# Performance work log

Hardware: AMD Instinct MI355X
Metric: run time of the kernel (lower is better)

The kernel has to match this reference:

```python
import jax, jax.numpy as jnp
import numpy as np

N_HEADS = 16


def setup_inputs() -> dict:
    key = jax.random.key(0)
    ks = jax.random.split(key, 7)
    B, S, D = 2, 2048, 1024
    x = jax.random.normal(ks[0], (B, S, D), dtype=jnp.float32)
    attn_mask = jax.random.normal(ks[1], (S, S), dtype=jnp.float32) * 0.1
    attn_bias = jax.random.normal(ks[2], (B, S, S), dtype=jnp.float32) * 0.1
    Wqkv = jax.random.normal(ks[3], (D, 3 * D), dtype=jnp.float32) * (D ** -0.5)
    bqkv = jnp.zeros((3 * D,), dtype=jnp.float32)
    Wout = jax.random.normal(ks[4], (D, D), dtype=jnp.float32) * (D ** -0.5)
    bout = jnp.zeros((D,), dtype=jnp.float32)
    return {"x": x, "attn_mask": attn_mask, "attn_bias": attn_bias,
            "Wqkv": Wqkv, "bqkv": bqkv, "Wout": Wout, "bout": bout}


def reference(x, attn_mask, attn_bias, Wqkv, bqkv, Wout, bout):
    B, S, D = x.shape
    H = N_HEADS
    hd = D // H
    # qkv projection: [B,S,3D] -> [3,B,H,S,hd]
    qkv = (x @ Wqkv + bqkv).reshape(B, S, 3, H, hd).transpose(2, 0, 3, 1, 4)
    q, k, v = qkv[0], qkv[1], qkv[2]
    scores = jnp.einsum('bhqd,bhkd->bhqk', q, k) / (hd ** 0.5)
    scores = scores + attn_mask[None, None, :, :] + attn_bias[:, None, :, :]
    attn = jax.nn.softmax(scores, axis=-1)  # dropout p=0.0 (eval)
    out = jnp.einsum('bhqk,bhkd->bhqd', attn, v)
    out = out.transpose(0, 2, 1, 3).reshape(B, S, D)
    return out @ Wout + bout
```

## Files before the change

### kernel.cpp

```cpp
#include <hip/hip_runtime.h>
#include <hip/hip_bf16.h>


#define S_LEN 2048
#define DMODEL 1024
#define NH 16
#define HD 64

typedef __bf16 bf16x8 __attribute__((ext_vector_type(8)));
typedef __bf16 bf16x4 __attribute__((ext_vector_type(4)));
typedef __bf16 bf16x2v __attribute__((ext_vector_type(2)));
typedef float f32x4 __attribute__((ext_vector_type(4)));
typedef short s16x4 __attribute__((ext_vector_type(4)));

#define GLD_LDS16(g, l)                                              \
  __builtin_amdgcn_global_load_lds(                                  \
      (const __attribute__((address_space(1))) unsigned int*)(g),    \
      (__attribute__((address_space(3))) unsigned int*)(l), 16, 0, 0)

#if __has_builtin(__builtin_amdgcn_mfma_f32_16x16x16bf16_1k)
#define HAVE_MFMA_16x16x16_BF16 1
#else
#define HAVE_MFMA_16x16x16_BF16 0
#endif

__global__ __launch_bounds__(256) void cvt_x(const float* __restrict__ X,
                                             __bf16* __restrict__ Xb) {
  int i = blockIdx.x * 256 + threadIdx.x;
  float4 v = ((const float4*)X)[i];
  bf16x4 o = {(__bf16)v.x, (__bf16)v.y, (__bf16)v.z, (__bf16)v.w};
  *(bf16x4*)&Xb[(size_t)i * 4] = o;
}

__global__ __launch_bounds__(256) void cvt_wt(const float* __restrict__ W,
                                              __bf16* __restrict__ Wt,
                                              int ncols) {
  __shared__ float tile[64][65];
  const int n0 = blockIdx.x * 64;
  const int k0 = blockIdx.y * 64;
  const int tid = threadIdx.x;
  {
    int c = tid & 63, r4 = tid >> 6;
#pragma unroll
    for (int p = 0; p < 16; ++p) {
      int r = r4 + p * 4;
      tile[r][c] = W[(size_t)(k0 + r) * ncols + n0 + c];
    }
  }
  __syncthreads();
  {
    int cc = (tid & 31) * 2, r8 = tid >> 5;
#pragma unroll
    for (int p = 0; p < 8; ++p) {
      int rr = r8 + p * 8;
      bf16x2v o = {(__bf16)tile[cc][rr], (__bf16)tile[cc + 1][rr]};
      *(bf16x2v*)&Wt[(size_t)(n0 + rr) * 1024 + k0 + cc] = o;
    }
  }
}

__global__ __launch_bounds__(256) void mb_fuse(const float* __restrict__ mask,
                                               const float* __restrict__ bias,
                                               __bf16* __restrict__ MB) {
  const int kt = blockIdx.x, qt = blockIdx.y, b = blockIdx.z;
  const int tid = threadIdx.x;
  const int w = tid >> 6, lane = tid & 63;
  const int quad = lane >> 4, c = lane & 15;
  const size_t qrow = (size_t)(qt * 64 + w * 16 + c);
  const int col0 = kt * 64 + quad * 4;
  const float* mp = mask + qrow * S_LEN + col0;
  const float* bp = bias + (size_t)b * S_LEN * S_LEN + qrow * S_LEN + col0;
  __bf16 vals[16];
#pragma unroll
  for (int ct = 0; ct < 4; ++ct) {
    float4 m = *(const float4*)(mp + ct * 16);
    float4 a = *(const float4*)(bp + ct * 16);
    vals[ct * 4 + 0] = (__bf16)(m.x + a.x);
    vals[ct * 4 + 1] = (__bf16)(m.y + a.y);
    vals[ct * 4 + 2] = (__bf16)(m.z + a.z);
    vals[ct * 4 + 3] = (__bf16)(m.w + a.w);
  }
  __bf16* op =
      MB + (((size_t)(b * 32 + qt) * 32 + kt) * 4096) + (w * 64 + lane) * 16;
  *(bf16x8*)op = *(bf16x8*)&vals[0];
  *(bf16x8*)(op + 8) = *(bf16x8*)&vals[8];
}

__global__ __launch_bounds__(256) void gemm_qkv_mfma(
    const __bf16* __restrict__ Xb, const __bf16* __restrict__ Wt,
    const float* __restrict__ bqkv, __bf16* __restrict__ Qb,
    __bf16* __restrict__ Kb, __bf16* __restrict__ Vtb) {
  __shared__ __align__(16) __bf16 As[128 * 32];
  __shared__ __align__(16) __bf16 Bs[128 * 32];
  const int tid = threadIdx.x;
  const int w = tid >> 6, lane = tid & 63;
  const int c = lane & 15, quad = lane >> 4;
  const int wm = w >> 1, wn = w & 1;
  const int rowBase = blockIdx.y * 128;
  const int colBase = blockIdx.x * 128;

  f32x4 acc[4][4] = {};

  const __bf16* gA0 =
      Xb + (size_t)(rowBase + w * 32 + (lane >> 2)) * 1024 + (lane & 3) * 8;
  const __bf16* gB0 =
      Wt + (size_t)(colBase + w * 32 + (lane >> 2)) * 1024 + (lane & 3) * 8;
  __bf16* lA0 = &As[(w * 32) * 32];
  __bf16* lB0 = &Bs[(w * 32) * 32];

  for (int k0 = 0; k0 < 1024; k0 += 32) {
    __syncthreads();
#pragma unroll
    for (int p = 0; p < 2; ++p) {
      GLD_LDS16(gA0 + (size_t)p * 16 * 1024 + k0, lA0 + p * 16 * 32);
      GLD_LDS16(gB0 + (size_t)p * 16 * 1024 + k0, lB0 + p * 16 * 32);
    }
    __syncthreads();

    bf16x8 af[4], bfr[4];
#pragma unroll
    for (int mt = 0; mt < 4; ++mt)
      af[mt] = *(const bf16x8*)&As[(wm * 64 + mt * 16 + c) * 32 + quad * 8];
#pragma unroll
    for (int nt = 0; nt < 4; ++nt)
      bfr[nt] = *(const bf16x8*)&Bs[(wn * 64 + nt * 16 + c) * 32 + quad * 8];
#pragma unroll
    for (int mt = 0; mt < 4; ++mt)
#pragma unroll
      for (int nt = 0; nt < 4; ++nt)
        acc[mt][nt] = __builtin_amdgcn_mfma_f32_16x16x32_bf16(
            af[mt], bfr[nt], acc[mt][nt], 0, 0, 0);
  }

#pragma unroll
  for (int mt = 0; mt < 4; ++mt) {
    int row0 = rowBase + wm * 64 + mt * 16 + quad * 4;
#pragma unroll
    for (int nt = 0; nt < 4; ++nt) {
      int col = colBase + wn * 64 + nt * 16 + c;
      float bias = bqkv[col];
      int three = col >> 10;
      int h = (col & 1023) >> 6;
      int d = col & 63;
#pragma unroll
      for (int r = 0; r < 4; ++r) {
        int rr = row0 + r;
        int bb = rr >> 11, s = rr & 2047;
        float val = acc[mt][nt][r] + bias;
        size_t ho = (size_t)(bb * NH + h);
        if (three == 0)
          Qb[(ho * S_LEN + s) * HD + d] = (__bf16)val;
        else if (three == 1)
          Kb[(ho * S_LEN + s) * HD + d] = (__bf16)val;
        else
          Vtb[(ho * HD + d) * S_LEN + s] = (__bf16)val;
      }
    }
  }
}

__global__ __launch_bounds__(256) void attn_mfma(
    const __bf16* __restrict__ Qb, const __bf16* __restrict__ Kb,
    const __bf16* __restrict__ Vtb, const __bf16* __restrict__ MB,
    __bf16* __restrict__ AOb) {
  const int qt = blockIdx.x, h = blockIdx.y, b = blockIdx.z;
  const int tid = threadIdx.x;
  const int w = tid >> 6;
  const int lane = tid & 63;
  const int c = lane & 15;
  const int quad = lane >> 4;

  __shared__ __align__(16) __bf16 Ks[2][64 * 64];
  __shared__ __align__(16) __bf16 Vs[2][64 * 64];
#if !HAVE_MFMA_16x16x16_BF16
  __shared__ __align__(16) __bf16 P2[4][16 * 72];
#endif

  const int qbase = qt * 64;
  const size_t headoff = (size_t)(b * NH + h) * S_LEN * HD;
  const __bf16* Qg = Qb + headoff + (size_t)qbase * HD;
  const __bf16* Kg = Kb + headoff;
  const __bf16* Vg = Vtb + headoff;
  const __bf16* MBg = MB + ((size_t)(b * 32 + qt) * 32) * 4096;

  const int f0 = tid >> 3, f1 = f0 + 32;
  const int j = tid & 7;
  const int sj0 = j ^ (f0 & 7);
  const int sj1 = j ^ (f1 & 7);
  const int lds0 = tid * 8;
  const int lds1 = (256 + tid) * 8;

  bf16x8 qa0 = *(const bf16x8*)(Qg + (w * 16 + c) * HD + quad * 8);
  bf16x8 qa1 = *(const bf16x8*)(Qg + (w * 16 + c) * HD + quad * 8 + 32);

  const int rs0 = (quad ^ (c & 7)) * 8;
  const int rs1 = ((quad + 4) ^ (c & 7)) * 8;

  f32x4 Oa[4] = {};
  float lsum = 0.f;

  GLD_LDS16(Kg + (size_t)f0 * HD + sj0 * 8, &Ks[0][lds0]);
  GLD_LDS16(Kg + (size_t)f1 * HD + sj1 * 8, &Ks[0][lds1]);
  GLD_LDS16(Vg + (size_t)f0 * S_LEN + sj0 * 8, &Vs[0][lds0]);
  GLD_LDS16(Vg + (size_t)f1 * S_LEN + sj1 * 8, &Vs[0][lds1]);
  __syncthreads();

  for (int kt = 0; kt < 32; ++kt) {
    const int cur = kt & 1, nxt = cur ^ 1;
    const __bf16* MBl = MBg + (size_t)kt * 4096 + (w * 64 + lane) * 16;
    bf16x8 rMB0 = *(const bf16x8*)MBl;
    bf16x8 rMB1 = *(const bf16x8*)(MBl + 8);
    if (kt < 31) {
      const int kb1 = (kt + 1) * 64;
      GLD_LDS16(Kg + (size_t)(kb1 + f0) * HD + sj0 * 8, &Ks[nxt][lds0]);
      GLD_LDS16(Kg + (size_t)(kb1 + f1) * HD + sj1 * 8, &Ks[nxt][lds1]);
      GLD_LDS16(Vg + (size_t)f0 * S_LEN + kb1 + sj0 * 8, &Vs[nxt][lds0]);
      GLD_LDS16(Vg + (size_t)f1 * S_LEN + kb1 + sj1 * 8, &Vs[nxt][lds1]);
    }

    f32x4 sv[4];
#pragma unroll
    for (int ct = 0; ct < 4; ++ct) {
      f32x4 a = {};
      bf16x8 kf0 = *(const bf16x8*)&Ks[cur][(ct * 16 + c) * 64 + rs0];
      bf16x8 kf1 = *(const bf16x8*)&Ks[cur][(ct * 16 + c) * 64 + rs1];
      a = __builtin_amdgcn_mfma_f32_16x16x32_bf16(kf0, qa0, a, 0, 0, 0);
      a = __builtin_amdgcn_mfma_f32_16x16x32_bf16(kf1, qa1, a, 0, 0, 0);
      sv[ct] = a;
    }
    s16x4 pb[4];
#pragma unroll
    for (int ct = 0; ct < 4; ++ct) {
      __bf16 t4[4];
#pragma unroll
      for (int r = 0; r < 4; ++r) {
        float mb = (ct < 2) ? (float)rMB0[ct * 4 + r]
                            : (float)rMB1[(ct - 2) * 4 + r];
        float p = __expf(sv[ct][r] * 0.125f + mb - 8.0f);
        lsum += p;
        t4[r] = (__bf16)p;
      }
      pb[ct] = *(s16x4*)t4;
    }

#if HAVE_MFMA_16x16x16_BF16
#pragma unroll
    for (int ft = 0; ft < 4; ++ft) {
      const int fr = ft * 16 + c;
#pragma unroll
      for (int ct = 0; ct < 4; ++ct) {
        const int chunk = ((ct * 2 + (quad >> 1)) ^ (fr & 7)) * 8 +
                          (quad & 1) * 4;
        s16x4 vf = *(const s16x4*)&Vs[cur][fr * 64 + chunk];
        Oa[ft] = __builtin_amdgcn_mfma_f32_16x16x16bf16_1k(vf, pb[ct],
                                                           Oa[ft], 0, 0, 0);
      }
    }
#else
#pragma unroll
    for (int ct = 0; ct < 4; ++ct)
      *(bf16x4*)&P2[w][c * 72 + ct * 16 + quad * 4] = *(bf16x4*)&pb[ct];
    bf16x8 pf0 = *(const bf16x8*)&P2[w][c * 72 + quad * 8];
    bf16x8 pf1 = *(const bf16x8*)&P2[w][c * 72 + 32 + quad * 8];
#pragma unroll
    for (int ft = 0; ft < 4; ++ft) {
      const int fr = ft * 16 + c;
      bf16x8 vf0 = *(const bf16x8*)&Vs[cur][fr * 64 + rs0];
      bf16x8 vf1 = *(const bf16x8*)&Vs[cur][fr * 64 + rs1];
      Oa[ft] =
          __builtin_amdgcn_mfma_f32_16x16x32_bf16(vf0, pf0, Oa[ft], 0, 0, 0);
      Oa[ft] =
          __builtin_amdgcn_mfma_f32_16x16x32_bf16(vf1, pf1, Oa[ft], 0, 0, 0);
    }
#endif

    __syncthreads();
  }
  lsum += __shfl_xor(lsum, 16);
  lsum += __shfl_xor(lsum, 32);
  const float invl = 1.0f / lsum;
  __bf16* orow =
      AOb + (size_t)(b * S_LEN + qbase + w * 16 + c) * DMODEL + h * HD;
#pragma unroll
  for (int ft = 0; ft < 4; ++ft) {
    __bf16 t4[4];
#pragma unroll
    for (int r = 0; r < 4; ++r) t4[r] = (__bf16)(Oa[ft][r] * invl);
    *(bf16x4*)(orow + ft * 16 + quad * 4) = *(bf16x4*)t4;
  }
}

__global__ __launch_bounds__(256) void gemm_out_mfma(
    const __bf16* __restrict__ AOb, const __bf16* __restrict__ Wt2,
    const float* __restrict__ bout, float* __restrict__ Out) {
  __shared__ __align__(16) __bf16 As[128 * 32];
  __shared__ __align__(16) __bf16 Bs[128 * 32];
  const int tid = threadIdx.x;
  const int w = tid >> 6, lane = tid & 63;
  const int c = lane & 15, quad = lane >> 4;
  const int wm = w >> 1, wn = w & 1;
  const int rowBase = blockIdx.y * 128;
  const int colBase = blockIdx.x * 128;

  f32x4 acc[4][4] = {};

  const __bf16* gA0 =
      AOb + (size_t)(rowBase + w * 32 + (lane >> 2)) * 1024 + (lane & 3) * 8;
  const __bf16* gB0 =
      Wt2 + (size_t)(colBase + w * 32 + (lane >> 2)) * 1024 + (lane & 3) * 8;
  __bf16* lA0 = &As[(w * 32) * 32];
  __bf16* lB0 = &Bs[(w * 32) * 32];

  for (int k0 = 0; k0 < 1024; k0 += 32) {
    __syncthreads();
#pragma unroll
    for (int p = 0; p < 2; ++p) {
      GLD_LDS16(gA0 + (size_t)p * 16 * 1024 + k0, lA0 + p * 16 * 32);
      GLD_LDS16(gB0 + (size_t)p * 16 * 1024 + k0, lB0 + p * 16 * 32);
    }
    __syncthreads();

    bf16x8 af[4], bfr[4];
#pragma unroll
    for (int mt = 0; mt < 4; ++mt)
      af[mt] = *(const bf16x8*)&As[(wm * 64 + mt * 16 + c) * 32 + quad * 8];
#pragma unroll
    for (int nt = 0; nt < 4; ++nt)
      bfr[nt] = *(const bf16x8*)&Bs[(wn * 64 + nt * 16 + c) * 32 + quad * 8];
#pragma unroll
    for (int mt = 0; mt < 4; ++mt)
#pragma unroll
      for (int nt = 0; nt < 4; ++nt)
        acc[mt][nt] = __builtin_amdgcn_mfma_f32_16x16x32_bf16(
            af[mt], bfr[nt], acc[mt][nt], 0, 0, 0);
  }

#pragma unroll
  for (int mt = 0; mt < 4; ++mt) {
    int row0 = rowBase + wm * 64 + mt * 16 + quad * 4;
#pragma unroll
    for (int nt = 0; nt < 4; ++nt) {
      int col = colBase + wn * 64 + nt * 16 + c;
      float bias = bout[col];
#pragma unroll
      for (int r = 0; r < 4; ++r)
        Out[(size_t)(row0 + r) * 1024 + col] = acc[mt][nt][r] + bias;
    }
  }
}

extern "C" void kernel_launch(void* const* d_in, const int* in_sizes, int n_in,
                              void* d_out, int out_size, void* d_ws,
                              size_t ws_size, hipStream_t stream) {
  const float* x = (const float*)d_in[0];
  const float* attn_mask = (const float*)d_in[1];
  const float* attn_bias = (const float*)d_in[2];
  const float* Wqkv = (const float*)d_in[3];
  const float* bqkv = (const float*)d_in[4];
  const float* Wout = (const float*)d_in[5];
  const float* bout = (const float*)d_in[6];
  float* out = (float*)d_out;

  __bf16* base = (__bf16*)d_ws;
  __bf16* Xb = base;
  __bf16* AOb = base;
  __bf16* Wt = base + 4194304;
  __bf16* Qb = base + 8388608;
  __bf16* Kb = base + 12582912;
  __bf16* Vtb = base + 16777216;
  __bf16* MB = base + 20971520;
  __bf16* Wt2 = base + 29360128;

  cvt_x<<<4096, 256, 0, stream>>>(x, Xb);
  cvt_wt<<<dim3(48, 16), 256, 0, stream>>>(Wqkv, Wt, 3072);
  cvt_wt<<<dim3(16, 16), 256, 0, stream>>>(Wout, Wt2, 1024);
  mb_fuse<<<dim3(32, 32, 2), 256, 0, stream>>>(attn_mask, attn_bias, MB);
  gemm_qkv_mfma<<<dim3(24, 32), 256, 0, stream>>>(Xb, Wt, bqkv, Qb, Kb, Vtb);
  attn_mfma<<<dim3(32, NH, 2), 256, 0, stream>>>(Qb, Kb, Vtb, MB, AOb);
  gemm_out_mfma<<<dim3(8, 32), 256, 0, stream>>>(AOb, Wt2, bout, out);
}
```

Before: 285.3 us.

## Use exp2 softmax, prefetch mask tile, coalesce mask fuse, shrink out-GEMM tile

The mask+bias fuse now reads row-coalesced float4 tiles into shared memory, pre-scales them by log2(e), and re-emits the MFMA fragment layout. Attention switches from __expf to the hardware exp2 with a folded scale constant, drops the -8 offset, prefetches the next mask tile into registers one iteration ahead, uses incremented K/V pointers, and vectorizes the partial-sum accumulation. The output GEMM moves from a 128x128 to a 128x64 tile, doubling the grid to 512 blocks for better CU occupancy at the cost of more A re-reads. Removing the -8 offset risks overflow only for large logits.

```diff
diff --git a/kernel.cpp b/kernel.cpp
--- a/kernel.cpp
+++ b/kernel.cpp
@@ -23,6 +23,18 @@
 #else
 #define HAVE_MFMA_16x16x16_BF16 0
 #endif
+
+#if __has_builtin(__builtin_amdgcn_exp2f)
+#define EXP2F(x) __builtin_amdgcn_exp2f(x)
+#else
+static __device__ __forceinline__ float EXP2F(float x) {
+  float r;
+  asm volatile("v_exp_f32 %0, %1" : "=v"(r) : "v"(x));
+  return r;
+}
+#endif
+
+#define LOG2E 1.44269504f
 
 __global__ __launch_bounds__(256) void cvt_x(const float* __restrict__ X,
                                              __bf16* __restrict__ Xb) {
@@ -64,21 +76,32 @@
                                                __bf16* __restrict__ MB) {
   const int kt = blockIdx.x, qt = blockIdx.y, b = blockIdx.z;
   const int tid = threadIdx.x;
+  __shared__ __bf16 sm[64][68];
+  {
+    const int r0 = tid >> 4;
+    const int cc = (tid & 15) * 4;
+    const float* mrow = mask + (size_t)(qt * 64) * S_LEN + kt * 64;
+    const float* brow =
+        bias + ((size_t)b * S_LEN + qt * 64) * S_LEN + kt * 64;
+#pragma unroll
+    for (int p = 0; p < 4; ++p) {
+      int r = r0 + p * 16;
+      float4 m = *(const float4*)(mrow + (size_t)r * S_LEN + cc);
+      float4 a = *(const float4*)(brow + (size_t)r * S_LEN + cc);
+      sm[r][cc + 0] = (__bf16)((m.x + a.x) * LOG2E);
+      sm[r][cc + 1] = (__bf16)((m.y + a.y) * LOG2E);
+      sm[r][cc + 2] = (__bf16)((m.z + a.z) * LOG2E);
+      sm[r][cc + 3] = (__bf16)((m.w + a.w) * LOG2E);
+    }
+  }
+  __syncthreads();
   const int w = tid >> 6, lane = tid & 63;
-  const int quad = lane >> 4, c = lane & 15;
-  const size_t qrow = (size_t)(qt * 64 + w * 16 + c);
-  const int col0 = kt * 64 + quad * 4;
-  const float* mp = mask + qrow * S_LEN + col0;
-  const float* bp = bias + (size_t)b * S_LEN * S_LEN + qrow * S_LEN + col0;
+  const int quad = lane >> 4, cl = lane & 15;
   __bf16 vals[16];
 #pragma unroll
   for (int ct = 0; ct < 4; ++ct) {
-    float4 m = *(const float4*)(mp + ct * 16);
-    float4 a = *(const float4*)(bp + ct * 16);
-    vals[ct * 4 + 0] = (__bf16)(m.x + a.x);
-    vals[ct * 4 + 1] = (__bf16)(m.y + a.y);
-    vals[ct * 4 + 2] = (__bf16)(m.z + a.z);
-    vals[ct * 4 + 3] = (__bf16)(m.w + a.w);
+    bf16x4 v = *(const bf16x4*)&sm[w * 16 + cl][ct * 16 + quad * 4];
+    *(bf16x4*)&vals[ct * 4] = v;
   }
   __bf16* op =
       MB + (((size_t)(b * 32 + qt) * 32 + kt) * 4096) + (w * 64 + lane) * 16;
@@ -197,26 +220,42 @@
   const int rs1 = ((quad + 4) ^ (c & 7)) * 8;
 
   f32x4 Oa[4] = {};
-  float lsum = 0.f;
+  f32x4 psum = {};
 
   GLD_LDS16(Kg + (size_t)f0 * HD + sj0 * 8, &Ks[0][lds0]);
   GLD_LDS16(Kg + (size_t)f1 * HD + sj1 * 8, &Ks[0][lds1]);
   GLD_LDS16(Vg + (size_t)f0 * S_LEN + sj0 * 8, &Vs[0][lds0]);
   GLD_LDS16(Vg + (size_t)f1 * S_LEN + sj1 * 8, &Vs[0][lds1]);
+
+  const __bf16* kgp0 = Kg + (size_t)(64 + f0) * HD + sj0 * 8;
+  const __bf16* kgp1 = Kg + (size_t)(64 + f1) * HD + sj1 * 8;
+  const __bf16* vgp0 = Vg + (size_t)f0 * S_LEN + 64 + sj0 * 8;
+  const __bf16* vgp1 = Vg + (size_t)f1 * S_LEN + 64 + sj1 * 8;
+
+  const __bf16* MBl = MBg + (w * 64 + lane) * 16;
+  bf16x8 rMB0 = *(const bf16x8*)MBl;
+  bf16x8 rMB1 = *(const bf16x8*)(MBl + 8);
+
   __syncthreads();
 
+  const float c1 = 0.125f * LOG2E;
+
+#pragma unroll 2
   for (int kt = 0; kt < 32; ++kt) {
     const int cur = kt & 1, nxt = cur ^ 1;
-    const __bf16* MBl = MBg + (size_t)kt * 4096 + (w * 64 + lane) * 16;
-    bf16x8 rMB0 = *(const bf16x8*)MBl;
-    bf16x8 rMB1 = *(const bf16x8*)(MBl + 8);
+    const __bf16* MBn = MBg + (size_t)(kt + 1) * 4096 + (w * 64 + lane) * 16;
+    bf16x8 nMB0 = *(const bf16x8*)MBn;
+    bf16x8 nMB1 = *(const bf16x8*)(MBn + 8);
     if (kt < 31) {
-      const int kb1 = (kt + 1) * 64;
-      GLD_LDS16(Kg + (size_t)(kb1 + f0) * HD + sj0 * 8, &Ks[nxt][lds0]);
-      GLD_LDS16(Kg + (size_t)(kb1 + f1) * HD + sj1 * 8, &Ks[nxt][lds1]);
-      GLD_LDS16(Vg + (size_t)f0 * S_LEN + kb1 + sj0 * 8, &Vs[nxt][lds0]);
-      GLD_LDS16(Vg + (size_t)f1 * S_LEN + kb1 + sj1 * 8, &Vs[nxt][lds1]);
-    }
+      GLD_LDS16(kgp0, &Ks[nxt][lds0]);
+      GLD_LDS16(kgp1, &Ks[nxt][lds1]);
+      GLD_LDS16(vgp0, &Vs[nxt][lds0]);
+      GLD_LDS16(vgp1, &Vs[nxt][lds1]);
+    }
+    kgp0 += 64 * HD;
+    kgp1 += 64 * HD;
+    vgp0 += 64;
+    vgp1 += 64;
 
     f32x4 sv[4];
 #pragma unroll
@@ -231,17 +270,21 @@
     s16x4 pb[4];
 #pragma unroll
     for (int ct = 0; ct < 4; ++ct) {
-      __bf16 t4[4];
+      f32x4 pv;
 #pragma unroll
       for (int r = 0; r < 4; ++r) {
         float mb = (ct < 2) ? (float)rMB0[ct * 4 + r]
                             : (float)rMB1[(ct - 2) * 4 + r];
-        float p = __expf(sv[ct][r] * 0.125f + mb - 8.0f);
-        lsum += p;
-        t4[r] = (__bf16)p;
+        pv[r] = EXP2F(sv[ct][r] * c1 + mb);
       }
+      psum += pv;
+      __bf16 t4[4];
+#pragma unroll
+      for (int r = 0; r < 4; ++r) t4[r] = (__bf16)pv[r];
       pb[ct] = *(s16x4*)t4;
     }
+    rMB0 = nMB0;
+    rMB1 = nMB1;
 
 #if HAVE_MFMA_16x16x16_BF16
 #pragma unroll
@@ -276,6 +319,7 @@
 
     __syncthreads();
   }
+  float lsum = psum[0] + psum[1] + psum[2] + psum[3];
   lsum += __shfl_xor(lsum, 16);
   lsum += __shfl_xor(lsum, 32);
   const float invl = 1.0f / lsum;
@@ -294,41 +338,39 @@
     const __bf16* __restrict__ AOb, const __bf16* __restrict__ Wt2,
     const float* __restrict__ bout, float* __restrict__ Out) {
   __shared__ __align__(16) __bf16 As[128 * 32];
-  __shared__ __align__(16) __bf16 Bs[128 * 32];
+  __shared__ __align__(16) __bf16 Bs[64 * 32];
   const int tid = threadIdx.x;
   const int w = tid >> 6, lane = tid & 63;
   const int c = lane & 15, quad = lane >> 4;
-  const int wm = w >> 1, wn = w & 1;
   const int rowBase = blockIdx.y * 128;
-  const int colBase = blockIdx.x * 128;
-
-  f32x4 acc[4][4] = {};
+  const int colBase = blockIdx.x * 64;
+
+  f32x4 acc[2][4] = {};
 
   const __bf16* gA0 =
       AOb + (size_t)(rowBase + w * 32 + (lane >> 2)) * 1024 + (lane & 3) * 8;
   const __bf16* gB0 =
-      Wt2 + (size_t)(colBase + w * 32 + (lane >> 2)) * 1024 + (lane & 3) * 8;
+      Wt2 + (size_t)(colBase + w * 16 + (lane >> 2)) * 1024 + (lane & 3) * 8;
   __bf16* lA0 = &As[(w * 32) * 32];
-  __bf16* lB0 = &Bs[(w * 32) * 32];
+  __bf16* lB0 = &Bs[(w * 16) * 32];
 
   for (int k0 = 0; k0 < 1024; k0 += 32) {
     __syncthreads();
 #pragma unroll
-    for (int p = 0; p < 2; ++p) {
+    for (int p = 0; p < 2; ++p)
       GLD_LDS16(gA0 + (size_t)p * 16 * 1024 + k0, lA0 + p * 16 * 32);
-      GLD_LDS16(gB0 + (size_t)p * 16 * 1024 + k0, lB0 + p * 16 * 32);
-    }
+    GLD_LDS16(gB0 + k0, lB0);
     __syncthreads();
 
-    bf16x8 af[4], bfr[4];
-#pragma unroll
-    for (int mt = 0; mt < 4; ++mt)
-      af[mt] = *(const bf16x8*)&As[(wm * 64 + mt * 16 + c) * 32 + quad * 8];
+    bf16x8 af[2], bfr[4];
+#pragma unroll
+    for (int mt = 0; mt < 2; ++mt)
+      af[mt] = *(const bf16x8*)&As[(w * 32 + mt * 16 + c) * 32 + quad * 8];
 #pragma unroll
     for (int nt = 0; nt < 4; ++nt)
-      bfr[nt] = *(const bf16x8*)&Bs[(wn * 64 + nt * 16 + c) * 32 + quad * 8];
-#pragma unroll
-    for (int mt = 0; mt < 4; ++mt)
+      bfr[nt] = *(const bf16x8*)&Bs[(nt * 16 + c) * 32 + quad * 8];
+#pragma unroll
+    for (int mt = 0; mt < 2; ++mt)
 #pragma unroll
       for (int nt = 0; nt < 4; ++nt)
         acc[mt][nt] = __builtin_amdgcn_mfma_f32_16x16x32_bf16(
@@ -336,11 +378,11 @@
   }
 
 #pragma unroll
-  for (int mt = 0; mt < 4; ++mt) {
-    int row0 = rowBase + wm * 64 + mt * 16 + quad * 4;
+  for (int mt = 0; mt < 2; ++mt) {
+    int row0 = rowBase + w * 32 + mt * 16 + quad * 4;
 #pragma unroll
     for (int nt = 0; nt < 4; ++nt) {
-      int col = colBase + wn * 64 + nt * 16 + c;
+      int col = colBase + nt * 16 + c;
       float bias = bout[col];
 #pragma unroll
       for (int r = 0; r < 4; ++r)
@@ -377,5 +419,5 @@
   mb_fuse<<<dim3(32, 32, 2), 256, 0, stream>>>(attn_mask, attn_bias, MB);
   gemm_qkv_mfma<<<dim3(24, 32), 256, 0, stream>>>(Xb, Wt, bqkv, Qb, Kb, Vtb);
   attn_mfma<<<dim3(32, NH, 2), 256, 0, stream>>>(Qb, Kb, Vtb, MB, AOb);
-  gemm_out_mfma<<<dim3(8, 32), 256, 0, stream>>>(AOb, Wt2, bout, out);
-}
+  gemm_out_mfma<<<dim3(16, 32), 256, 0, stream>>>(AOb, Wt2, bout, out);
+}
```

New measurement: 285.1 us. No clear change (-0.1%).
